# Kernel tuning notes

Measured on AMD Instinct MI355X. Metric: run time of the kernel, lower is better.

## Reference

```python
import jax, jax.numpy as jnp
import numpy as np

N_POL, N_TICK, N_COMM = 1000, 98000, 1000
N = N_POL + N_TICK + N_COMM
E = 1000000
EMB, HID, OUT, HEADS = 32, 64, 32, 4
EDGE_DIM = 5
N_STATES, N_SECTORS, N_INDUSTRIES = 50, 11, 74


def _p(k, shape, fan_in):
    return jax.random.normal(k, shape, jnp.float32) * (1.0 / np.sqrt(fan_in))


def setup_inputs():
    ks = jax.random.split(jax.random.key(0), 30)
    F1 = HID // HEADS
    d = {}
    d["edge_index"] = jax.random.randint(ks[0], (2, E), 0, N)
    d["edge_attr"] = jax.random.normal(ks[1], (E, EDGE_DIM), jnp.float32)
    d["pol_feat"] = jax.random.normal(ks[2], (N_POL, 7), jnp.float32)
    d["state_ids"] = jax.random.randint(ks[3], (N_POL,), 0, N_STATES)
    d["sector_ids"] = jax.random.randint(ks[4], (N_TICK,), 0, N_SECTORS)
    d["industry_ids"] = jax.random.randint(ks[5], (N_TICK,), 0, N_INDUSTRIES)
    d["comp_scalar"] = jax.random.normal(ks[6], (N_TICK, 1), jnp.float32)
    d["pol_W"] = _p(ks[7], (7, EMB), 7); d["pol_b"] = jnp.zeros((EMB,), jnp.float32)
    d["state_E"] = _p(ks[8], (N_STATES, EMB), 1)
    d["sector_E"] = _p(ks[9], (N_SECTORS, 8), 1)
    d["industry_E"] = _p(ks[10], (N_INDUSTRIES, 8), 1)
    d["comp_W"] = _p(ks[11], (17, EMB), 17); d["comp_b"] = jnp.zeros((EMB,), jnp.float32)
    d["comm_E"] = _p(ks[12], (N_COMM, EMB), 1)
    d["ln_g"] = jnp.ones((EMB,), jnp.float32); d["ln_b"] = jnp.zeros((EMB,), jnp.float32)
    d["c1_W"] = _p(ks[13], (EMB, HEADS * F1), EMB)
    d["c1_as"] = _p(ks[14], (HEADS, F1), F1); d["c1_ad"] = _p(ks[15], (HEADS, F1), F1)
    d["c1_eW"] = _p(ks[16], (EDGE_DIM, HEADS * F1), EDGE_DIM)
    d["c1_ae"] = _p(ks[17], (HEADS, F1), F1)
    d["c1_b"] = jnp.zeros((HID,), jnp.float32)
    d["c2_W"] = _p(ks[18], (HID, OUT), HID)
    d["c2_as"] = _p(ks[19], (1, OUT), OUT); d["c2_ad"] = _p(ks[20], (1, OUT), OUT)
    d["c2_eW"] = _p(ks[21], (EDGE_DIM, OUT), EDGE_DIM)
    d["c2_ae"] = _p(ks[22], (1, OUT), OUT)
    d["c2_b"] = jnp.zeros((OUT,), jnp.float32)
    return d


def _segment_softmax(logits, seg, num):
    # numerically stable per-destination softmax, per head (axis 0 is edges)
    m = jax.ops.segment_max(logits, seg, num_segments=num)
    ex = jnp.exp(logits - m[seg])
    s = jax.ops.segment_sum(ex, seg, num_segments=num)
    return ex / s[seg]


def _gat(x, src, dst, eattr, W, a_s, a_d, eW, a_e, b, heads, feat, concat):
    # PyG GATConv (eval mode): linear -> per-node alpha terms -> per-edge
    # leaky_relu -> destination softmax -> weighted scatter-sum.
    n = x.shape[0]
    h = (x @ W).reshape(n, heads, feat)                     # [N,H,F]
    a_src = jnp.sum(h * a_s, -1)                            # [N,H]
    a_dst = jnp.sum(h * a_d, -1)                            # [N,H]
    a_edge = jnp.sum((eattr @ eW).reshape(-1, heads, feat) * a_e, -1)  # [E,H]
    alpha = jax.nn.leaky_relu(a_src[src] + a_dst[dst] + a_edge, 0.2)
    alpha = _segment_softmax(alpha, dst, n)                 # [E,H]
    out = jax.ops.segment_sum(h[src] * alpha[..., None], dst, num_segments=n)
    out = out.reshape(n, heads * feat) if concat else out.mean(1)
    return out + b


def _forward(edge_index, edge_attr, pol_feat, state_ids, sector_ids, industry_ids,
             comp_scalar, pol_W, pol_b, state_E, sector_E, industry_E, comp_W,
             comp_b, comm_E, ln_g, ln_b, c1_W, c1_as, c1_ad, c1_eW, c1_ae, c1_b,
             c2_W, c2_as, c2_ad, c2_eW, c2_ae, c2_b):
    # node features
    pol = jax.nn.relu(pol_feat @ pol_W + pol_b) + state_E[state_ids]
    comp_in = jnp.concatenate([sector_E[sector_ids], industry_E[industry_ids], comp_scalar], 1)
    comp = jax.nn.relu(comp_in @ comp_W + comp_b)
    x = jnp.concatenate([pol, comp, comm_E], 0)             # [N,EMB]
    mu = jnp.mean(x, -1, keepdims=True)
    var = jnp.mean((x - mu) ** 2, -1, keepdims=True)
    x = (x - mu) / jnp.sqrt(var + 1e-5) * ln_g + ln_b
    # add self-loops with fill_value='mean' (per-dst mean of incoming edge_attr)
    src, dst = edge_index[0], edge_index[1]
    cnt = jax.ops.segment_sum(jnp.ones((E,), jnp.float32), dst, num_segments=N)
    loop_attr = jax.ops.segment_sum(edge_attr, dst, num_segments=N) / jnp.maximum(cnt, 1.0)[:, None]
    idx = jnp.arange(N)
    src2 = jnp.concatenate([src, idx]); dst2 = jnp.concatenate([dst, idx])
    ea2 = jnp.concatenate([edge_attr, loop_attr], 0)
    x = jax.nn.elu(_gat(x, src2, dst2, ea2, c1_W, c1_as, c1_ad, c1_eW, c1_ae, c1_b, HEADS, HID // HEADS, True))
    x = _gat(x, src2, dst2, ea2, c2_W, c2_as, c2_ad, c2_eW, c2_ae, c2_b, 1, OUT, False)
    return x


def reference(edge_index, edge_attr, pol_feat, state_ids, sector_ids, industry_ids,
              comp_scalar, pol_W, pol_b, state_E, sector_E, industry_E, comp_W,
              comp_b, comm_E, ln_g, ln_b, c1_W, c1_as, c1_ad, c1_eW, c1_ae, c1_b,
              c2_W, c2_as, c2_ad, c2_eW, c2_ae, c2_b):
    return _forward(edge_index, edge_attr, pol_feat, state_ids, sector_ids, industry_ids,
                    comp_scalar, pol_W, pol_b, state_E, sector_E, industry_E, comp_W,
                    comp_b, comm_E, ln_g, ln_b, c1_W, c1_as, c1_ad, c1_eW, c1_ae, c1_b,
                    c2_W, c2_as, c2_ad, c2_eW, c2_ae, c2_b)
```

## Files before the change

### kernel.cpp

```cpp
#include <hip/hip_runtime.h>
#include <math.h>

#define NPOL   1000
#define NTICK  98000
#define NCOMM  1000
#define NN     100000
#define NE     1000000
#define NFEATBLK 1563

#define BKTSHIFT 9
#define NBKT     196
#define BKTCAP   6144
#define KA_EPB   4096
#define KA_BLOCKS 245

__device__ __forceinline__ unsigned short f2bf(float v) {
    unsigned u = __float_as_uint(v);
    u += 0x7FFFu + ((u >> 16) & 1u);
    return (unsigned short)(u >> 16);
}
__device__ __forceinline__ float bf2f(unsigned short s) {
    return __uint_as_float(((unsigned)s) << 16);
}

__global__ void __launch_bounds__(256) k_feat(
    const float* __restrict__ pol_feat, const int* __restrict__ state_ids,
    const int* __restrict__ sector_ids, const int* __restrict__ industry_ids,
    const float* __restrict__ comp_scalar,
    const float* __restrict__ pol_W, const float* __restrict__ pol_b,
    const float* __restrict__ state_E, const float* __restrict__ sector_E,
    const float* __restrict__ industry_E, const float* __restrict__ comp_W,
    const float* __restrict__ comp_b, const float* __restrict__ comm_E,
    const float* __restrict__ ln_g, const float* __restrict__ ln_b,
    const float* __restrict__ c1_W, const float* __restrict__ c1_as,
    const float* __restrict__ c1_ad,
    unsigned short* __restrict__ h1b, float* __restrict__ as1,
    float* __restrict__ ad1) {
    __shared__ float sW1[2048];
    __shared__ float sCompW[544];
    __shared__ float sPolW[224];
    __shared__ float sAs[64], sAd[64];
    __shared__ float sLg[32], sLb[32], sPb[32], sCb[32];
    int t = threadIdx.x;
    for (int i = t; i < 2048; i += 256) sW1[i] = c1_W[i];
    for (int i = t; i < 544; i += 256) sCompW[i] = comp_W[i];
    if (t < 224) sPolW[t] = pol_W[t];
    if (t < 64) { sAs[t] = c1_as[t]; sAd[t] = c1_ad[t]; }
    if (t < 32) { sLg[t] = ln_g[t]; sLb[t] = ln_b[t]; sPb[t] = pol_b[t]; sCb[t] = comp_b[t]; }
    __syncthreads();
    int tid = blockIdx.x * 256 + t;
    if (tid >= 4 * NN) return;
    int n = tid >> 2, q = tid & 3, jb = q * 8;
    float x[8];
    if (n < NPOL) {
        float f[7];
        #pragma unroll
        for (int i = 0; i < 7; ++i) f[i] = pol_feat[n * 7 + i];
        int sid = state_ids[n];
        #pragma unroll
        for (int jj = 0; jj < 8; ++jj) {
            int j = jb + jj;
            float v = sPb[j];
            #pragma unroll
            for (int i = 0; i < 7; ++i) v += f[i] * sPolW[i * 32 + j];
            v = v > 0.f ? v : 0.f;
            x[jj] = v + state_E[sid * 32 + j];
        }
    } else if (n < NPOL + NTICK) {
        int tt = n - NPOL;
        float f[17];
        int sec = sector_ids[tt], ind = industry_ids[tt];
        #pragma unroll
        for (int i = 0; i < 8; ++i) { f[i] = sector_E[sec * 8 + i]; f[8 + i] = industry_E[ind * 8 + i]; }
        f[16] = comp_scalar[tt];
        #pragma unroll
        for (int jj = 0; jj < 8; ++jj) {
            int j = jb + jj;
            float v = sCb[j];
            #pragma unroll
            for (int i = 0; i < 17; ++i) v += f[i] * sCompW[i * 32 + j];
            x[jj] = v > 0.f ? v : 0.f;
        }
    } else {
        int c = n - (NPOL + NTICK);
        float4 a = *(const float4*)&comm_E[c * 32 + jb];
        float4 b = *(const float4*)&comm_E[c * 32 + jb + 4];
        x[0] = a.x; x[1] = a.y; x[2] = a.z; x[3] = a.w;
        x[4] = b.x; x[5] = b.y; x[6] = b.z; x[7] = b.w;
    }
    float s1 = 0.f;
    #pragma unroll
    for (int jj = 0; jj < 8; ++jj) s1 += x[jj];
    s1 += __shfl_xor(s1, 1); s1 += __shfl_xor(s1, 2);
    float mu = s1 * (1.f / 32.f);
    float s2 = 0.f;
    #pragma unroll
    for (int jj = 0; jj < 8; ++jj) { float dd = x[jj] - mu; s2 += dd * dd; }
    s2 += __shfl_xor(s2, 1); s2 += __shfl_xor(s2, 2);
    float inv = rsqrtf(s2 * (1.f / 32.f) + 1e-5f);
    #pragma unroll
    for (int jj = 0; jj < 8; ++jj) x[jj] = (x[jj] - mu) * inv * sLg[jb + jj] + sLb[jb + jj];
    float4 acc0 = {0,0,0,0}, acc1 = {0,0,0,0}, acc2 = {0,0,0,0}, acc3 = {0,0,0,0};
    int qb = (t & 63) & ~3;
    int jc = q * 16;
    #pragma unroll
    for (int p = 0; p < 4; ++p) {
        #pragma unroll
        for (int jj = 0; jj < 8; ++jj) {
            float xs = __shfl(x[jj], qb + p, 64);
            const float4* wr = (const float4*)&sW1[(p * 8 + jj) * 64 + jc];
            float4 w0 = wr[0], w1 = wr[1], w2 = wr[2], w3 = wr[3];
            acc0.x = fmaf(xs, w0.x, acc0.x); acc0.y = fmaf(xs, w0.y, acc0.y);
            acc0.z = fmaf(xs, w0.z, acc0.z); acc0.w = fmaf(xs, w0.w, acc0.w);
            acc1.x = fmaf(xs, w1.x, acc1.x); acc1.y = fmaf(xs, w1.y, acc1.y);
            acc1.z = fmaf(xs, w1.z, acc1.z); acc1.w = fmaf(xs, w1.w, acc1.w);
            acc2.x = fmaf(xs, w2.x, acc2.x); acc2.y = fmaf(xs, w2.y, acc2.y);
            acc2.z = fmaf(xs, w2.z, acc2.z); acc2.w = fmaf(xs, w2.w, acc2.w);
            acc3.x = fmaf(xs, w3.x, acc3.x); acc3.y = fmaf(xs, w3.y, acc3.y);
            acc3.z = fmaf(xs, w3.z, acc3.z); acc3.w = fmaf(xs, w3.w, acc3.w);
        }
    }
    const float4* asv = (const float4*)sAs;
    const float4* adv = (const float4*)sAd;
    float4 a0 = asv[q * 4], a1 = asv[q * 4 + 1], a2 = asv[q * 4 + 2], a3 = asv[q * 4 + 3];
    float4 b0 = adv[q * 4], b1v = adv[q * 4 + 1], b2v = adv[q * 4 + 2], b3 = adv[q * 4 + 3];
    float av = acc0.x * a0.x + acc0.y * a0.y + acc0.z * a0.z + acc0.w * a0.w
             + acc1.x * a1.x + acc1.y * a1.y + acc1.z * a1.z + acc1.w * a1.w
             + acc2.x * a2.x + acc2.y * a2.y + acc2.z * a2.z + acc2.w * a2.w
             + acc3.x * a3.x + acc3.y * a3.y + acc3.z * a3.z + acc3.w * a3.w;
    float dv = acc0.x * b0.x + acc0.y * b0.y + acc0.z * b0.z + acc0.w * b0.w
             + acc1.x * b1v.x + acc1.y * b1v.y + acc1.z * b1v.z + acc1.w * b1v.w
             + acc2.x * b2v.x + acc2.y * b2v.y + acc2.z * b2v.z + acc2.w * b2v.w
             + acc3.x * b3.x + acc3.y * b3.y + acc3.z * b3.z + acc3.w * b3.w;
    as1[tid] = av;
    ad1[tid] = dv;
    uint4 w1o, w2o;
    w1o.x = (unsigned)f2bf(acc0.x) | ((unsigned)f2bf(acc0.y) << 16);
    w1o.y = (unsigned)f2bf(acc0.z) | ((unsigned)f2bf(acc0.w) << 16);
    w1o.z = (unsigned)f2bf(acc1.x) | ((unsigned)f2bf(acc1.y) << 16);
    w1o.w = (unsigned)f2bf(acc1.z) | ((unsigned)f2bf(acc1.w) << 16);
    w2o.x = (unsigned)f2bf(acc2.x) | ((unsigned)f2bf(acc2.y) << 16);
    w2o.y = (unsigned)f2bf(acc2.z) | ((unsigned)f2bf(acc2.w) << 16);
    w2o.z = (unsigned)f2bf(acc3.x) | ((unsigned)f2bf(acc3.y) << 16);
    w2o.w = (unsigned)f2bf(acc3.z) | ((unsigned)f2bf(acc3.w) << 16);
    unsigned short* hp = h1b + (unsigned)n * 64u + (unsigned)jc;
    *(uint4*)hp = w1o;
    *(uint4*)(hp + 8) = w2o;
}

__global__ void __launch_bounds__(1024) k_bucket(
    const int* __restrict__ ei, const float* __restrict__ edge_attr,
    const float* __restrict__ c1_eW, const float* __restrict__ c1_ae,
    const float* __restrict__ c2_eW, const float* __restrict__ c2_ae,
    int* __restrict__ bucket_cnt, float4* __restrict__ bucketbuf) {
    __shared__ float we1s[20];
    __shared__ float we2s[5];
    __shared__ int hcnt[NBKT];
    __shared__ int hbase[NBKT];
    int t = threadIdx.x;
    if (t < 20) {
        int d = t >> 2, h = t & 3;
        float s = 0.f;
        for (int f = 0; f < 16; ++f) s += c1_eW[d * 64 + h * 16 + f] * c1_ae[h * 16 + f];
        we1s[t] = s;
    } else if (t >= 32 && t < 37) {
        int d = t - 32;
        float s = 0.f;
        for (int f = 0; f < 32; ++f) s += c2_eW[d * 32 + f] * c2_ae[f];
        we2s[d] = s;
    }
    if (t < NBKT) hcnt[t] = 0;
    __syncthreads();
    int e0 = blockIdx.x * KA_EPB + t;
    int bk[4], rk[4];
    float4 rec[4];
    #pragma unroll
    for (int k = 0; k < 4; ++k) {
        int e = e0 + k * 1024;
        bk[k] = -1;
        if (e < NE) {
            int s = ei[e];
            int d = ei[NE + e];
            int bkt = d >> BKTSHIFT;
            int dl = d & ((1 << BKTSHIFT) - 1);
            float a[5];
            #pragma unroll
            for (int kk = 0; kk < 5; ++kk) a[kk] = edge_attr[e * 5 + kk];
            float v0 = 0.f, v1 = 0.f, v2 = 0.f, v3 = 0.f, v4 = 0.f;
            #pragma unroll
            for (int kk = 0; kk < 5; ++kk) {
                v0 += a[kk] * we1s[kk * 4 + 0];
                v1 += a[kk] * we1s[kk * 4 + 1];
                v2 += a[kk] * we1s[kk * 4 + 2];
                v3 += a[kk] * we1s[kk * 4 + 3];
                v4 += a[kk] * we2s[kk];
            }
            unsigned u01 = (unsigned)f2bf(v0) | ((unsigned)f2bf(v1) << 16);
            unsigned u23 = (unsigned)f2bf(v2) | ((unsigned)f2bf(v3) << 16);
            unsigned pk = (unsigned)s | ((unsigned)dl << 17);
            rec[k] = make_float4(__uint_as_float(pk), __uint_as_float(u01),
                                 __uint_as_float(u23), v4);
            bk[k] = bkt;
            rk[k] = atomicAdd(&hcnt[bkt], 1);
        }
    }
    __syncthreads();
    if (t < NBKT && hcnt[t] > 0) hbase[t] = atomicAdd(&bucket_cnt[t * 16], hcnt[t]);
    __syncthreads();
    #pragma unroll
    for (int k = 0; k < 4; ++k) {
        if (bk[k] >= 0) {
            int pos = hbase[bk[k]] + rk[k];
            if (pos < BKTCAP)
                bucketbuf[(size_t)bk[k] * BKTCAP + pos] = rec[k];
        }
    }
}

__global__ void __launch_bounds__(1024) k_sortfill(
    const int* __restrict__ bucket_cnt, const float4* __restrict__ bucketbuf,
    float4* __restrict__ rec2, int* __restrict__ deg, int* __restrict__ erow) {
    __shared__ int pref[256];
    __shared__ int hist[512];
    __shared__ int hoff[512];
    int t = threadIdx.x;
    int b = blockIdx.x;
    if (t < 256) pref[t] = (t < NBKT) ? bucket_cnt[t * 16] : 0;
    if (t < 512) hist[t] = 0;
    __syncthreads();
    for (int off = 1; off < 256; off <<= 1) {
        int v = 0;
        if (t < 256 && t >= off) v = pref[t - off];
        __syncthreads();
        if (t < 256) pref[t] += v;
        __syncthreads();
    }
    int count = bucket_cnt[b * 16];
    if (count > BKTCAP) count = BKTCAP;
    int region = (b == 0) ? 0 : pref[b - 1];
    float4 rv[6];
    int dlv[6], rrv[6];
    #pragma unroll
    for (int k = 0; k < 6; ++k) {
        int i = k * 1024 + t;
        dlv[k] = -1;
        if (i < count) {
            float4 p = bucketbuf[(size_t)b * BKTCAP + i];
            int dl = (int)(__float_as_uint(p.x) >> 17);
            p.x = __uint_as_float(__float_as_uint(p.x) & 0x1FFFFu);
            rv[k] = p;
            dlv[k] = dl;
            rrv[k] = atomicAdd(&hist[dl], 1);
        }
    }
    __syncthreads();
    if (t < 512) hoff[t] = hist[t];
    __syncthreads();
    for (int off = 1; off < 512; off <<= 1) {
        int v = 0;
        if (t < 512 && t >= off) v = hoff[t - off];
        __syncthreads();
        if (t < 512) hoff[t] += v;
        __syncthreads();
    }
    #pragma unroll
    for (int k = 0; k < 6; ++k) {
        if (dlv[k] >= 0) {
            int pos = region + hoff[dlv[k]] - hist[dlv[k]] + rrv[k];
            rec2[pos] = rv[k];
        }
    }
    int n = (b << BKTSHIFT) + t;
    if (t < 512 && n < NN) {
        deg[n] = hist[t];
        erow[n] = region + hoff[t] - hist[t];
    }
}

__global__ void __launch_bounds__(256) k_agg1(
    const int* __restrict__ erow, const int* __restrict__ deg,
    const float4* __restrict__ rec2,
    const float* __restrict__ as1, const float* __restrict__ ad1,
    const unsigned short* __restrict__ h1b, const float* __restrict__ c1_b,
    unsigned short* __restrict__ x1b, float* __restrict__ selfae2) {
    __shared__ float pT[4][2][32][4];
    __shared__ int   srcT[4][2][32];
    int wid = threadIdx.x >> 6;
    int lane = threadIdx.x & 63;
    int half = lane >> 5;
    int j = lane & 31;
    int h = j >> 3;
    int n = blockIdx.x * 8 + wid * 2 + half;
    int base = erow[n];
    int dg   = deg[n];
    const float4* as1v4 = (const float4*)as1;
    const float4* ad1v4 = (const float4*)ad1;
    float4 adv = ad1v4[n];
    float4 asv = as1v4[n];
    unsigned uself = *(const unsigned*)(h1b + (unsigned)n * 64u + 2u * (unsigned)j);

    float ssum = 0.f, acc0 = 0.f, acc1 = 0.f;
    float aes0 = 0.f, aes1 = 0.f, aes2 = 0.f, aes3 = 0.f, ae2sum = 0.f;

    for (int i0 = 0; i0 < dg; i0 += 32) {
        int clen = dg - i0; if (clen > 32) clen = 32;
        int idx = i0 + j;
        if (idx < dg) {
            float4 r = rec2[base + idx];
            int s = __float_as_int(r.x);
            unsigned u01 = __float_as_uint(r.y), u23 = __float_as_uint(r.z);
            float ae0  = bf2f((unsigned short)u01);
            float ae1v = bf2f((unsigned short)(u01 >> 16));
            float ae2v = bf2f((unsigned short)u23);
            float ae3v = bf2f((unsigned short)(u23 >> 16));
            float4 av = as1v4[s];
            float l0 = av.x + adv.x + ae0;  l0 = l0 > 0.f ? l0 : 0.2f * l0;
            float l1 = av.y + adv.y + ae1v; l1 = l1 > 0.f ? l1 : 0.2f * l1;
            float l2 = av.z + adv.z + ae2v; l2 = l2 > 0.f ? l2 : 0.2f * l2;
            float l3 = av.w + adv.w + ae3v; l3 = l3 > 0.f ? l3 : 0.2f * l3;
            float4 q = make_float4(__expf(l0), __expf(l1), __expf(l2), __expf(l3));
            *(float4*)&pT[wid][half][j][0] = q;
            srcT[wid][half][j] = s;
            aes0 += ae0; aes1 += ae1v; aes2 += ae2v; aes3 += ae3v;
            ae2sum += r.w;
        }
        int i = 0;
        for (; i + 4 <= clen; i += 4) {
            int s0 = srcT[wid][half][i],     s1 = srcT[wid][half][i + 1];
            int s2 = srcT[wid][half][i + 2], s3 = srcT[wid][half][i + 3];
            float q0 = pT[wid][half][i][h],     q1 = pT[wid][half][i + 1][h];
            float q2 = pT[wid][half][i + 2][h], q3 = pT[wid][half][i + 3][h];
            unsigned g0 = *(const unsigned*)(h1b + (unsigned)s0 * 64u + 2u * (unsigned)j);
            unsigned g1 = *(const unsigned*)(h1b + (unsigned)s1 * 64u + 2u * (unsigned)j);
            unsigned g2 = *(const unsigned*)(h1b + (unsigned)s2 * 64u + 2u * (unsigned)j);
            unsigned g3 = *(const unsigned*)(h1b + (unsigned)s3 * 64u + 2u * (unsigned)j);
            ssum += (q0 + q1) + (q2 + q3);
            acc0 = fmaf(q0, bf2f((unsigned short)g0),
                   fmaf(q1, bf2f((unsigned short)g1),
                   fmaf(q2, bf2f((unsigned short)g2),
                   fmaf(q3, bf2f((unsigned short)g3), acc0))));
            acc1 = fmaf(q0, bf2f((unsigned short)(g0 >> 16)),
                   fmaf(q1, bf2f((unsigned short)(g1 >> 16)),
                   fmaf(q2, bf2f((unsigned short)(g2 >> 16)),
                   fmaf(q3, bf2f((unsigned short)(g3 >> 16)), acc1))));
        }
        for (; i < clen; ++i) {
            int s0 = srcT[wid][half][i];
            float q0 = pT[wid][half][i][h];
            unsigned g0 = *(const unsigned*)(h1b + (unsigned)s0 * 64u + 2u * (unsigned)j);
            ssum += q0;
            acc0 = fmaf(q0, bf2f((unsigned short)g0), acc0);
            acc1 = fmaf(q0, bf2f((unsigned short)(g0 >> 16)), acc1);
        }
    }
    #pragma unroll
    for (int m = 1; m < 32; m <<= 1) {
        aes0 += __shfl_xor(aes0, m);
        aes1 += __shfl_xor(aes1, m);
        aes2 += __shfl_xor(aes2, m);
        aes3 += __shfl_xor(aes3, m);
        ae2sum += __shfl_xor(ae2sum, m);
    }
    float invd = 1.f / fmaxf((float)dg, 1.f);
    float aesh = (h == 0) ? aes0 : (h == 1) ? aes1 : (h == 2) ? aes2 : aes3;
    float adh  = (h == 0) ? adv.x : (h == 1) ? adv.y : (h == 2) ? adv.z : adv.w;
    float ash  = (h == 0) ? asv.x : (h == 1) ? asv.y : (h == 2) ? asv.z : asv.w;
    float ls = ash + adh + aesh * invd;
    ls = ls > 0.f ? ls : 0.2f * ls;
    float ps = __expf(ls);
    ssum += ps;
    acc0 = fmaf(ps, bf2f((unsigned short)uself), acc0);
    acc1 = fmaf(ps, bf2f((unsigned short)(uself >> 16)), acc1);
    if (lane == 0) selfae2[n] = ae2sum * invd;
    if (lane == 32) selfae2[n] = ae2sum * invd;
    float inv_s = 1.f / ssum;
    float x0 = acc0 * inv_s + c1_b[2 * j];
    float x1 = acc1 * inv_s + c1_b[2 * j + 1];
    x0 = (x0 > 0.f) ? x0 : (__expf(x0) - 1.f);
    x1 = (x1 > 0.f) ? x1 : (__expf(x1) - 1.f);
    unsigned w = (unsigned)f2bf(x0) | ((unsigned)f2bf(x1) << 16);
    *(unsigned*)(x1b + (unsigned)n * 64u + 2u * (unsigned)j) = w;
}

__global__ void __launch_bounds__(256) k_mid(
    const unsigned short* __restrict__ x1b, const float* __restrict__ c2_W,
    const float* __restrict__ c2_as, const float* __restrict__ c2_ad,
    unsigned short* __restrict__ h2b, float* __restrict__ as2,
    float* __restrict__ ad2) {
    int wave = (blockIdx.x * 256 + threadIdx.x) >> 6;
    int lane = threadIdx.x & 63;
    int half = lane >> 5, j = lane & 31;
    int n = wave * 2 + half;
    unsigned u = *(const unsigned*)(x1b + (unsigned)n * 64u + j * 2u);
    float acc = 0.f;
    #pragma unroll
    for (int t = 0; t < 32; ++t) {
        unsigned xu = (unsigned)__shfl((int)u, half * 32 + t, 64);
        float x0 = bf2f((unsigned short)xu);
        float x1 = bf2f((unsigned short)(xu >> 16));
        acc = fmaf(x0, c2_W[(2 * t) * 32 + j], acc);
        acc = fmaf(x1, c2_W[(2 * t + 1) * 32 + j], acc);
    }
    float a = acc * c2_as[j], b = acc * c2_ad[j];
    #pragma unroll
    for (int m = 16; m > 0; m >>= 1) {
        a += __shfl_xor(a, m, 64);
        b += __shfl_xor(b, m, 64);
    }
    if (j == 0) { as2[n] = a; ad2[n] = b; }
    h2b[(unsigned)n * 32u + j] = f2bf(acc);
}

__global__ void __launch_bounds__(256) k_agg2(
    const int* __restrict__ erow, const int* __restrict__ deg,
    const float4* __restrict__ rec2, const float* __restrict__ as2,
    const float* __restrict__ ad2, const float* __restrict__ selfae2,
    const unsigned short* __restrict__ h2b, const float* __restrict__ c2_b,
    float* __restrict__ out) {
    __shared__ float2 spT[8][32];
    int t = threadIdx.x;
    int half = t >> 5;
    int l32 = t & 31;
    int n = blockIdx.x * 8 + half;
    int base = erow[n];
    int dg = deg[n];
    float ad2n = ad2[n];
    float ssum = 0.f, acc = 0.f;
    for (int i0 = 0; i0 < dg; i0 += 32) {
        int clen = dg - i0; if (clen > 32) clen = 32;
        int idx = i0 + l32;
        float p = 0.f; int s = 0;
        if (idx < dg) {
            float4 r = rec2[base + idx];
            s = __float_as_int(r.x);
            float l = as2[s] + ad2n + r.w;
            l = l > 0.f ? l : 0.2f * l;
            p = __expf(l);
        }
        ssum += p;
        spT[half][l32] = make_float2(__int_as_float(s), p);
        int i = 0;
        for (; i + 4 <= clen; i += 4) {
            float2 e0 = spT[half][i],     e1 = spT[half][i + 1];
            float2 e2 = spT[half][i + 2], e3 = spT[half][i + 3];
            int s0 = __float_as_int(e0.x), s1 = __float_as_int(e1.x);
            int s2 = __float_as_int(e2.x), s3 = __float_as_int(e3.x);
            float g0 = bf2f(h2b[(unsigned)s0 * 32u + l32]);
            float g1 = bf2f(h2b[(unsigned)s1 * 32u + l32]);
            float g2 = bf2f(h2b[(unsigned)s2 * 32u + l32]);
            float g3 = bf2f(h2b[(unsigned)s3 * 32u + l32]);
            acc = fmaf(e0.y, g0, fmaf(e1.y, g1, fmaf(e2.y, g2, fmaf(e3.y, g3, acc))));
        }
        for (; i < clen; ++i) {
            float2 e0 = spT[half][i];
            int s0 = __float_as_int(e0.x);
            acc = fmaf(e0.y, bf2f(h2b[(unsigned)s0 * 32u + l32]), acc);
        }
    }
    #pragma unroll
    for (int m = 1; m < 32; m <<= 1) ssum += __shfl_xor(ssum, m, 32);
    float ls = as2[n] + ad2n + selfae2[n];
    ls = ls > 0.f ? ls : 0.2f * ls;
    float ps = __expf(ls);
    ssum += ps;
    acc = fmaf(ps, bf2f(h2b[(unsigned)n * 32u + l32]), acc);
    out[(size_t)n * 32 + l32] = acc / ssum + c2_b[l32];
}

extern "C" void kernel_launch(void* const* d_in, const int* in_sizes, int n_in,
                              void* d_out, int out_size, void* d_ws, size_t ws_size,
                              hipStream_t stream) {
    const int*   edge_index  = (const int*)  d_in[0];
    const float* edge_attr   = (const float*)d_in[1];
    const float* pol_feat    = (const float*)d_in[2];
    const int*   state_ids   = (const int*)  d_in[3];
    const int*   sector_ids  = (const int*)  d_in[4];
    const int*   industry_ids= (const int*)  d_in[5];
    const float* comp_scalar = (const float*)d_in[6];
    const float* pol_W   = (const float*)d_in[7];
    const float* pol_b   = (const float*)d_in[8];
    const float* state_E = (const float*)d_in[9];
    const float* sector_E= (const float*)d_in[10];
    const float* industry_E=(const float*)d_in[11];
    const float* comp_W  = (const float*)d_in[12];
    const float* comp_b  = (const float*)d_in[13];
    const float* comm_E  = (const float*)d_in[14];
    const float* ln_g    = (const float*)d_in[15];
    const float* ln_b    = (const float*)d_in[16];
    const float* c1_W    = (const float*)d_in[17];
    const float* c1_as   = (const float*)d_in[18];
    const float* c1_ad   = (const float*)d_in[19];
    const float* c1_eW   = (const float*)d_in[20];
    const float* c1_ae   = (const float*)d_in[21];
    const float* c1_b    = (const float*)d_in[22];
    const float* c2_W    = (const float*)d_in[23];
    const float* c2_as   = (const float*)d_in[24];
    const float* c2_ad   = (const float*)d_in[25];
    const float* c2_eW   = (const float*)d_in[26];
    const float* c2_ae   = (const float*)d_in[27];
    const float* c2_b    = (const float*)d_in[28];
    float* out = (float*)d_out;

    char* ws = (char*)d_ws;
    size_t off = 0;
    auto alloc = [&](size_t bytes) { void* p = ws + off; off += (bytes + 255) & ~(size_t)255; return p; };
    int*    bucket_cnt = (int*)   alloc((size_t)NBKT * 16 * 4);
    float4* bucketbuf  = (float4*)alloc((size_t)NBKT * BKTCAP * 16);
    float4* rec2       = (float4*)alloc((size_t)NE * 16);
    int*    deg        = (int*)   alloc(NN * 4);
    int*    erow       = (int*)   alloc(NN * 4);
    float*  selfae2    = (float*) alloc(NN * 4);
    unsigned short* h1b = (unsigned short*)alloc((size_t)NN * 64 * 2);
    float* as1       = (float*)alloc((size_t)NN * 4 * 4);
    float* ad1       = (float*)alloc((size_t)NN * 4 * 4);
    unsigned short* x1b = (unsigned short*)alloc((size_t)NN * 64 * 2);
    unsigned short* h2b = (unsigned short*)alloc((size_t)NN * 32 * 2);
    float* as2       = (float*)alloc(NN * 4);
    float* ad2       = (float*)alloc(NN * 4);
    (void)ws_size; (void)in_sizes; (void)n_in; (void)out_size;

    hipMemsetAsync(bucket_cnt, 0, (size_t)NBKT * 16 * 4, stream);

    k_feat<<<NFEATBLK, 256, 0, stream>>>(
        pol_feat, state_ids, sector_ids, industry_ids, comp_scalar,
        pol_W, pol_b, state_E, sector_E, industry_E, comp_W, comp_b, comm_E,
        ln_g, ln_b, c1_W, c1_as, c1_ad, h1b, as1, ad1);
    k_bucket<<<KA_BLOCKS, 1024, 0, stream>>>(
        edge_index, edge_attr, c1_eW, c1_ae, c2_eW, c2_ae, bucket_cnt, bucketbuf);
    k_sortfill<<<NBKT, 1024, 0, stream>>>(
        bucket_cnt, bucketbuf, rec2, deg, erow);
    k_agg1<<<NN / 8, 256, 0, stream>>>(
        erow, deg, rec2, as1, ad1, h1b, c1_b, x1b, selfae2);
    k_mid<<<(NN / 2) / 4, 256, 0, stream>>>(
        x1b, c2_W, c2_as, c2_ad, h2b, as2, ad2);
    k_agg2<<<NN / 8, 256, 0, stream>>>(
        erow, deg, rec2, as2, ad2, selfae2, h2b, c2_b, out);
}
```

Baseline: 175.4 us.

## Fuse feature and bucket kernels, fold mid projection into layer-1 aggregation

```diff
diff --git a/kernel.cpp b/kernel.cpp
--- a/kernel.cpp
+++ b/kernel.cpp
@@ -6,13 +6,13 @@
 #define NCOMM  1000
 #define NN     100000
 #define NE     1000000
-#define NFEATBLK 1563
 
 #define BKTSHIFT 9
 #define NBKT     196
 #define BKTCAP   6144
 #define KA_EPB   4096
 #define KA_BLOCKS 245
+#define FEATBLKS  391
 
 __device__ __forceinline__ unsigned short f2bf(float v) {
     unsigned u = __float_as_uint(v);
@@ -23,7 +23,15 @@
     return __uint_as_float(((unsigned)s) << 16);
 }
 
-__global__ void __launch_bounds__(256) k_feat(
+__global__ void k_zero(int* __restrict__ bucket_cnt) {
+    for (int i = threadIdx.x; i < NBKT * 16; i += 1024) bucket_cnt[i] = 0;
+}
+
+__global__ void __launch_bounds__(1024) k_featbucket(
+    const int* __restrict__ ei, const float* __restrict__ edge_attr,
+    const float* __restrict__ c1_eW, const float* __restrict__ c1_ae,
+    const float* __restrict__ c2_eW, const float* __restrict__ c2_ae,
+    int* __restrict__ bucket_cnt, float4* __restrict__ bucketbuf,
     const float* __restrict__ pol_feat, const int* __restrict__ state_ids,
     const int* __restrict__ sector_ids, const int* __restrict__ industry_ids,
     const float* __restrict__ comp_scalar,
@@ -36,19 +44,86 @@
     const float* __restrict__ c1_ad,
     unsigned short* __restrict__ h1b, float* __restrict__ as1,
     float* __restrict__ ad1) {
+    int t = threadIdx.x;
+    if (blockIdx.x < KA_BLOCKS) {
+        __shared__ float we1s[20];
+        __shared__ float we2s[5];
+        __shared__ int hcnt[NBKT];
+        __shared__ int hbase[NBKT];
+        if (t < 20) {
+            int d = t >> 2, h = t & 3;
+            float s = 0.f;
+            for (int f = 0; f < 16; ++f) s += c1_eW[d * 64 + h * 16 + f] * c1_ae[h * 16 + f];
+            we1s[t] = s;
+        } else if (t >= 32 && t < 37) {
+            int d = t - 32;
+            float s = 0.f;
+            for (int f = 0; f < 32; ++f) s += c2_eW[d * 32 + f] * c2_ae[f];
+            we2s[d] = s;
+        }
+        if (t < NBKT) hcnt[t] = 0;
+        __syncthreads();
+        int e0 = blockIdx.x * KA_EPB + t;
+        int bk[4], rk[4];
+        float4 rec[4];
+        #pragma unroll
+        for (int k = 0; k < 4; ++k) {
+            int e = e0 + k * 1024;
+            bk[k] = -1;
+            if (e < NE) {
+                int s = ei[e];
+                int d = ei[NE + e];
+                int bkt = d >> BKTSHIFT;
+                int dl = d & ((1 << BKTSHIFT) - 1);
+                float a[5];
+                #pragma unroll
+                for (int kk = 0; kk < 5; ++kk) a[kk] = edge_attr[e * 5 + kk];
+                float v0 = 0.f, v1 = 0.f, v2 = 0.f, v3 = 0.f, v4 = 0.f;
+                #pragma unroll
+                for (int kk = 0; kk < 5; ++kk) {
+                    v0 += a[kk] * we1s[kk * 4 + 0];
+                    v1 += a[kk] * we1s[kk * 4 + 1];
+                    v2 += a[kk] * we1s[kk * 4 + 2];
+                    v3 += a[kk] * we1s[kk * 4 + 3];
+                    v4 += a[kk] * we2s[kk];
+                }
+                unsigned u01 = (unsigned)f2bf(v0) | ((unsigned)f2bf(v1) << 16);
+                unsigned u23 = (unsigned)f2bf(v2) | ((unsigned)f2bf(v3) << 16);
+                unsigned pk = (unsigned)s | ((unsigned)dl << 17);
+                rec[k] = make_float4(__uint_as_float(pk), __uint_as_float(u01),
+                                     __uint_as_float(u23), v4);
+                bk[k] = bkt;
+                rk[k] = atomicAdd(&hcnt[bkt], 1);
+            }
+        }
+        __syncthreads();
+        if (t < NBKT && hcnt[t] > 0) hbase[t] = atomicAdd(&bucket_cnt[t * 16], hcnt[t]);
+        __syncthreads();
+        #pragma unroll
+        for (int k = 0; k < 4; ++k) {
+            if (bk[k] >= 0) {
+                int pos = hbase[bk[k]] + rk[k];
+                if (pos < BKTCAP)
+                    bucketbuf[(size_t)bk[k] * BKTCAP + pos] = rec[k];
+            }
+        }
+        return;
+    }
     __shared__ float sW1[2048];
     __shared__ float sCompW[544];
     __shared__ float sPolW[224];
     __shared__ float sAs[64], sAd[64];
     __shared__ float sLg[32], sLb[32], sPb[32], sCb[32];
-    int t = threadIdx.x;
-    for (int i = t; i < 2048; i += 256) sW1[i] = c1_W[i];
-    for (int i = t; i < 544; i += 256) sCompW[i] = comp_W[i];
-    if (t < 224) sPolW[t] = pol_W[t];
-    if (t < 64) { sAs[t] = c1_as[t]; sAd[t] = c1_ad[t]; }
-    if (t < 32) { sLg[t] = ln_g[t]; sLb[t] = ln_b[t]; sPb[t] = pol_b[t]; sCb[t] = comp_b[t]; }
+    for (int i = t; i < 2048; i += 1024) sW1[i] = c1_W[i];
+    if (t < 544) sCompW[t] = comp_W[t];
+    if (t >= 544 && t < 768) sPolW[t - 544] = pol_W[t - 544];
+    if (t >= 768 && t < 832) { sAs[t - 768] = c1_as[t - 768]; sAd[t - 768] = c1_ad[t - 768]; }
+    if (t >= 832 && t < 864) {
+        int i = t - 832;
+        sLg[i] = ln_g[i]; sLb[i] = ln_b[i]; sPb[i] = pol_b[i]; sCb[i] = comp_b[i];
+    }
     __syncthreads();
-    int tid = blockIdx.x * 256 + t;
+    int tid = (blockIdx.x - KA_BLOCKS) * 1024 + t;
     if (tid >= 4 * NN) return;
     int n = tid >> 2, q = tid & 3, jb = q * 8;
     float x[8];
@@ -148,75 +223,6 @@
     *(uint4*)(hp + 8) = w2o;
 }
 
-__global__ void __launch_bounds__(1024) k_bucket(
-    const int* __restrict__ ei, const float* __restrict__ edge_attr,
-    const float* __restrict__ c1_eW, const float* __restrict__ c1_ae,
-    const float* __restrict__ c2_eW, const float* __restrict__ c2_ae,
-    int* __restrict__ bucket_cnt, float4* __restrict__ bucketbuf) {
-    __shared__ float we1s[20];
-    __shared__ float we2s[5];
-    __shared__ int hcnt[NBKT];
-    __shared__ int hbase[NBKT];
-    int t = threadIdx.x;
-    if (t < 20) {
-        int d = t >> 2, h = t & 3;
-        float s = 0.f;
-        for (int f = 0; f < 16; ++f) s += c1_eW[d * 64 + h * 16 + f] * c1_ae[h * 16 + f];
-        we1s[t] = s;
-    } else if (t >= 32 && t < 37) {
-        int d = t - 32;
-        float s = 0.f;
-        for (int f = 0; f < 32; ++f) s += c2_eW[d * 32 + f] * c2_ae[f];
-        we2s[d] = s;
-    }
-    if (t < NBKT) hcnt[t] = 0;
-    __syncthreads();
-    int e0 = blockIdx.x * KA_EPB + t;
-    int bk[4], rk[4];
-    float4 rec[4];
-    #pragma unroll
-    for (int k = 0; k < 4; ++k) {
-        int e = e0 + k * 1024;
-        bk[k] = -1;
-        if (e < NE) {
-            int s = ei[e];
-            int d = ei[NE + e];
-            int bkt = d >> BKTSHIFT;
-            int dl = d & ((1 << BKTSHIFT) - 1);
-            float a[5];
-            #pragma unroll
-            for (int kk = 0; kk < 5; ++kk) a[kk] = edge_attr[e * 5 + kk];
-            float v0 = 0.f, v1 = 0.f, v2 = 0.f, v3 = 0.f, v4 = 0.f;
-            #pragma unroll
-            for (int kk = 0; kk < 5; ++kk) {
-                v0 += a[kk] * we1s[kk * 4 + 0];
-                v1 += a[kk] * we1s[kk * 4 + 1];
-                v2 += a[kk] * we1s[kk * 4 + 2];
-                v3 += a[kk] * we1s[kk * 4 + 3];
-                v4 += a[kk] * we2s[kk];
-            }
-            unsigned u01 = (unsigned)f2bf(v0) | ((unsigned)f2bf(v1) << 16);
-            unsigned u23 = (unsigned)f2bf(v2) | ((unsigned)f2bf(v3) << 16);
-            unsigned pk = (unsigned)s | ((unsigned)dl << 17);
-            rec[k] = make_float4(__uint_as_float(pk), __uint_as_float(u01),
-                                 __uint_as_float(u23), v4);
-            bk[k] = bkt;
-            rk[k] = atomicAdd(&hcnt[bkt], 1);
-        }
-    }
-    __syncthreads();
-    if (t < NBKT && hcnt[t] > 0) hbase[t] = atomicAdd(&bucket_cnt[t * 16], hcnt[t]);
-    __syncthreads();
-    #pragma unroll
-    for (int k = 0; k < 4; ++k) {
-        if (bk[k] >= 0) {
-            int pos = hbase[bk[k]] + rk[k];
-            if (pos < BKTCAP)
-                bucketbuf[(size_t)bk[k] * BKTCAP + pos] = rec[k];
-        }
-    }
-}
-
 __global__ void __launch_bounds__(1024) k_sortfill(
     const int* __restrict__ bucket_cnt, const float4* __restrict__ bucketbuf,
     float4* __restrict__ rec2, int* __restrict__ deg, int* __restrict__ erow) {
@@ -277,12 +283,15 @@
     }
 }
 
-__global__ void __launch_bounds__(256) k_agg1(
+__global__ void __launch_bounds__(256) k_agg1m(
     const int* __restrict__ erow, const int* __restrict__ deg,
     const float4* __restrict__ rec2,
     const float* __restrict__ as1, const float* __restrict__ ad1,
     const unsigned short* __restrict__ h1b, const float* __restrict__ c1_b,
-    unsigned short* __restrict__ x1b, float* __restrict__ selfae2) {
+    const float* __restrict__ c2_W, const float* __restrict__ c2_as,
+    const float* __restrict__ c2_ad,
+    unsigned short* __restrict__ h2b, float* __restrict__ as2,
+    float* __restrict__ ad2, float* __restrict__ selfae2) {
     __shared__ float pT[4][2][32][4];
     __shared__ int   srcT[4][2][32];
     int wid = threadIdx.x >> 6;
@@ -379,27 +388,14 @@
     x0 = (x0 > 0.f) ? x0 : (__expf(x0) - 1.f);
     x1 = (x1 > 0.f) ? x1 : (__expf(x1) - 1.f);
     unsigned w = (unsigned)f2bf(x0) | ((unsigned)f2bf(x1) << 16);
-    *(unsigned*)(x1b + (unsigned)n * 64u + 2u * (unsigned)j) = w;
-}
-
-__global__ void __launch_bounds__(256) k_mid(
-    const unsigned short* __restrict__ x1b, const float* __restrict__ c2_W,
-    const float* __restrict__ c2_as, const float* __restrict__ c2_ad,
-    unsigned short* __restrict__ h2b, float* __restrict__ as2,
-    float* __restrict__ ad2) {
-    int wave = (blockIdx.x * 256 + threadIdx.x) >> 6;
-    int lane = threadIdx.x & 63;
-    int half = lane >> 5, j = lane & 31;
-    int n = wave * 2 + half;
-    unsigned u = *(const unsigned*)(x1b + (unsigned)n * 64u + j * 2u);
     float acc = 0.f;
     #pragma unroll
-    for (int t = 0; t < 32; ++t) {
-        unsigned xu = (unsigned)__shfl((int)u, half * 32 + t, 64);
-        float x0 = bf2f((unsigned short)xu);
-        float x1 = bf2f((unsigned short)(xu >> 16));
-        acc = fmaf(x0, c2_W[(2 * t) * 32 + j], acc);
-        acc = fmaf(x1, c2_W[(2 * t + 1) * 32 + j], acc);
+    for (int tt = 0; tt < 32; ++tt) {
+        unsigned xu = (unsigned)__shfl((int)w, half * 32 + tt, 64);
+        float xa = bf2f((unsigned short)xu);
+        float xb = bf2f((unsigned short)(xu >> 16));
+        acc = fmaf(xa, c2_W[(2 * tt) * 32 + j], acc);
+        acc = fmaf(xb, c2_W[(2 * tt + 1) * 32 + j], acc);
     }
     float a = acc * c2_as[j], b = acc * c2_ad[j];
     #pragma unroll
@@ -513,26 +509,22 @@
     unsigned short* h1b = (unsigned short*)alloc((size_t)NN * 64 * 2);
     float* as1       = (float*)alloc((size_t)NN * 4 * 4);
     float* ad1       = (float*)alloc((size_t)NN * 4 * 4);
-    unsigned short* x1b = (unsigned short*)alloc((size_t)NN * 64 * 2);
     unsigned short* h2b = (unsigned short*)alloc((size_t)NN * 32 * 2);
     float* as2       = (float*)alloc(NN * 4);
     float* ad2       = (float*)alloc(NN * 4);
     (void)ws_size; (void)in_sizes; (void)n_in; (void)out_size;
 
-    hipMemsetAsync(bucket_cnt, 0, (size_t)NBKT * 16 * 4, stream);
-
-    k_feat<<<NFEATBLK, 256, 0, stream>>>(
+    k_zero<<<1, 1024, 0, stream>>>(bucket_cnt);
+    k_featbucket<<<KA_BLOCKS + FEATBLKS, 1024, 0, stream>>>(
+        edge_index, edge_attr, c1_eW, c1_ae, c2_eW, c2_ae, bucket_cnt, bucketbuf,
         pol_feat, state_ids, sector_ids, industry_ids, comp_scalar,
         pol_W, pol_b, state_E, sector_E, industry_E, comp_W, comp_b, comm_E,
         ln_g, ln_b, c1_W, c1_as, c1_ad, h1b, as1, ad1);
-    k_bucket<<<KA_BLOCKS, 1024, 0, stream>>>(
-        edge_index, edge_attr, c1_eW, c1_ae, c2_eW, c2_ae, bucket_cnt, bucketbuf);
     k_sortfill<<<NBKT, 1024, 0, stream>>>(
         bucket_cnt, bucketbuf, rec2, deg, erow);
-    k_agg1<<<NN / 8, 256, 0, stream>>>(
-        erow, deg, rec2, as1, ad1, h1b, c1_b, x1b, selfae2);
-    k_mid<<<(NN / 2) / 4, 256, 0, stream>>>(
-        x1b, c2_W, c2_as, c2_ad, h2b, as2, ad2);
+    k_agg1m<<<NN / 8, 256, 0, stream>>>(
+        erow, deg, rec2, as1, ad1, h1b, c1_b, c2_W, c2_as, c2_ad,
+        h2b, as2, ad2, selfae2);
     k_agg2<<<NN / 8, 256, 0, stream>>>(
         erow, deg, rec2, as2, ad2, selfae2, h2b, c2_b, out);
 }
```

New measurement: 159.3 us, median of 3. -9.2%, faster.
